# Kernel tuning notes

Measured on AMD Instinct MI355X. Metric: run time of the kernel, lower is better.

## Reference

```python
import jax, jax.numpy as jnp
import numpy as np

N = 20000
E = 320000
IN_C = 256
HID = 64
OUT_C = 64
NUM_LAYERS = 3
HEADS = 8


def setup_inputs() -> dict:
    key = jax.random.key(0)
    ks = jax.random.split(key, 12)
    s_in = 1.0 / np.sqrt(IN_C)
    s_h = 1.0 / np.sqrt(HID)
    inp = {
        "x": jax.random.normal(ks[0], (N, IN_C), dtype=jnp.float32),
        "edge_index": jax.random.randint(ks[1], (2, E), 0, N, dtype=jnp.int64),
        "lin1_w": jax.random.uniform(ks[2], (IN_C, HID), jnp.float32, -s_in, s_in),
        "lin1_b": jnp.zeros((HID,), jnp.float32),
        "wq": jax.random.uniform(ks[3], (NUM_LAYERS, HID, HID), jnp.float32, -s_h, s_h),
        "bq": jnp.zeros((NUM_LAYERS, HID), jnp.float32),
        "wk": jax.random.uniform(ks[4], (NUM_LAYERS, HID, HID), jnp.float32, -s_h, s_h),
        "bk": jnp.zeros((NUM_LAYERS, HID), jnp.float32),
        "wv": jax.random.uniform(ks[5], (NUM_LAYERS, HID, HID), jnp.float32, -s_h, s_h),
        "bv": jnp.zeros((NUM_LAYERS, HID), jnp.float32),
        "lin2_w": jax.random.uniform(ks[6], (HID, OUT_C), jnp.float32, -s_h, s_h),
        "lin2_b": jnp.zeros((OUT_C,), jnp.float32),
    }
    return inp


def reference(x, edge_index, lin1_w, lin1_b, wq, bq, wk, bk, wv, bv, lin2_w, lin2_b):
    n = x.shape[0]
    C = lin1_w.shape[1]
    d = C // HEADS  # per-head dim
    inv_sqrt_d = 1.0 / (d ** 0.5)

    # gcn_norm with self-loops (symmetric normalization, edge weights = 1)
    loop = jnp.arange(n, dtype=edge_index.dtype)
    row = jnp.concatenate([edge_index[0], loop])  # source j
    col = jnp.concatenate([edge_index[1], loop])  # target i
    deg = jax.ops.segment_sum(jnp.ones_like(col, dtype=x.dtype), col, num_segments=n)
    dinv = jnp.where(deg > 0, deg ** -0.5, 0.0)
    norm = dinv[row] * dinv[col]  # [E+N]

    # input projection (dropout inactive in eval mode)
    h = jax.nn.relu(x @ lin1_w + lin1_b)
    x_all = h[:, None, :]  # [N, 1, C] growing history

    for l in range(NUM_LAYERS):
        t = x_all.shape[1]
        # node-level projections (linear commutes with gather)
        q = x_all[:, -1] @ wq[l] + bq[l]                      # [N, C]
        k = jnp.einsum("ntc,cd->ntd", x_all, wk[l]) + bk[l]   # [N, t, C]
        v = jnp.einsum("ntc,cd->ntd", x_all, wv[l]) + bv[l]   # [N, t, C]
        # per-edge multi-head attention of target's latest repr over source history
        Qe = q[col].reshape(-1, HEADS, d)                      # [E', H, d]
        Ke = k[row].reshape(-1, t, HEADS, d)                   # [E', t, H, d]
        Ve = v[row].reshape(-1, t, HEADS, d)
        scores = jnp.einsum("ehd,ethd->eht", Qe, Ke) * inv_sqrt_d
        attn = jax.nn.softmax(scores, axis=-1)                 # [E', H, t]
        msg = jnp.einsum("eht,ethd->ehd", attn, Ve).reshape(-1, C)
        msg = msg * norm[:, None]
        out = jax.ops.segment_sum(msg, col, num_segments=n)    # sum aggregation
        out = jax.nn.relu(out)
        x_all = jnp.concatenate([x_all, out[:, None, :]], axis=1)

    logits = x_all[:, -1] @ lin2_w + lin2_b
    return jax.nn.log_softmax(logits, axis=1)
```

## Files before the change

### kernel.cpp

```cpp
#include <hip/hip_runtime.h>
#include <math.h>

#define HID 64
#define HEADS 8
#define ALD 72

typedef __attribute__((ext_vector_type(8))) short bf16x8;
typedef __attribute__((ext_vector_type(4))) float f32x4;

__device__ __forceinline__ unsigned short f2bf(float f) {
    union { float f; unsigned int u; } cv; cv.f = f;
    unsigned int u = cv.u;
    unsigned int r = (u + 0x7FFFu + ((u >> 16) & 1u)) >> 16;
    return (unsigned short)r;
}
__device__ __forceinline__ float bflo(unsigned int u) {
    union { unsigned int u; float f; } cv; cv.u = u << 16; return cv.f;
}
__device__ __forceinline__ float bfhi(unsigned int u) {
    union { unsigned int u; float f; } cv; cv.u = u & 0xFFFF0000u; return cv.f;
}
__device__ __forceinline__ unsigned relu_pk(unsigned u) {
    unsigned m = ((u & 0x8000u) ? 0u : 0xFFFFu) |
                 ((u & 0x80000000u) ? 0u : 0xFFFF0000u);
    return u & m;
}

__device__ __forceinline__ float dot2bf(unsigned a, unsigned b, float c) {
    float d;
    asm("v_dot2_f32_bf16 %0, %1, %2, %3" : "=v"(d) : "v"(a), "v"(b), "v"(c));
    return d;
}

__global__ void k_count(const int* __restrict__ col, int* __restrict__ counts, int E) {
    int e = blockIdx.x * blockDim.x + threadIdx.x;
    if (e < E) atomicAdd(&counts[col[e]], 1);
}

__device__ __forceinline__ void scan256_body(const int* __restrict__ counts,
                                             int* __restrict__ start,
                                             float* __restrict__ dinv, int n,
                                             int tid, int* sscan) {
    int lane = tid & 63, wvi = tid >> 6;
    int ipt = (n + 255) >> 8;
    int c0 = tid * ipt;
    int c1 = min(n, c0 + ipt);
    if (c0 > n) c0 = n;
    int s = 0;
    for (int i = c0; i < c1; ++i) s += counts[i];
    int x = s;
#pragma unroll
    for (int off = 1; off < 64; off <<= 1) {
        int y = __shfl_up(x, off);
        if (lane >= off) x += y;
    }
    if (lane == 63) sscan[wvi] = x;
    __syncthreads();
    if (tid == 0) {
        int r = 0;
#pragma unroll
        for (int i = 0; i < 4; ++i) { int t = sscan[i]; sscan[i + 4] = r; r += t; }
        start[n] = r;
    }
    __syncthreads();
    int run = sscan[wvi + 4] + (x - s);
    for (int i = c0; i < c1; ++i) {
        int v = counts[i];
        start[i] = run;
        dinv[i] = rsqrtf((float)(v + 1));
        run += v;
    }
}

__device__ __forceinline__ void stage_w_bf16(unsigned short* Wt,
                                             const float* __restrict__ w, int tid) {
    for (int idx = tid; idx < 1024; idx += 256) {
        int k = idx >> 4, n4 = (idx & 15) * 4;
        float4 wv = *(const float4*)&w[k * 64 + n4];
        Wt[(n4 + 0) * ALD + k] = f2bf(wv.x);
        Wt[(n4 + 1) * ALD + k] = f2bf(wv.y);
        Wt[(n4 + 2) * ALD + k] = f2bf(wv.z);
        Wt[(n4 + 3) * ALD + k] = f2bf(wv.w);
    }
}

__device__ __forceinline__ void mfma_step(const unsigned short* Alds,
                                          const unsigned short* Wt,
                                          int tid, f32x4 acc[4]) {
    int lane = tid & 63;
    int m0 = (tid >> 6) * 16;
    int c16 = lane & 15, quad = lane >> 4;
    const unsigned short* ar = &Alds[(m0 + c16) * ALD + quad * 8];
    bf16x8 a0 = *(const bf16x8*)ar;
    bf16x8 a1 = *(const bf16x8*)(ar + 32);
#pragma unroll
    for (int nt = 0; nt < 4; ++nt) {
        const unsigned short* br = &Wt[(nt * 16 + c16) * ALD + quad * 8];
        bf16x8 b0 = *(const bf16x8*)br;
        bf16x8 b1 = *(const bf16x8*)(br + 32);
        acc[nt] = __builtin_amdgcn_mfma_f32_16x16x32_bf16(a0, b0, acc[nt], 0, 0, 0);
        acc[nt] = __builtin_amdgcn_mfma_f32_16x16x32_bf16(a1, b1, acc[nt], 0, 0, 0);
    }
}

__device__ __forceinline__ void stage_tile_body(
    const unsigned short* __restrict__ src, const float* __restrict__ w,
    const float* __restrict__ b, float* __restrict__ qd,
    unsigned short* __restrict__ kvdst, int kv_stride, int kv_off, bool relu_in,
    int node0, int n, int tid, unsigned short* Alds, unsigned short* Wt) {
    stage_w_bf16(Wt, w, tid);
    for (int idx = tid; idx < 512; idx += 256) {
        int r = idx >> 3, seg = idx & 7;
        int node = node0 + r;
        uint4 u = make_uint4(0u, 0u, 0u, 0u);
        if (node < n) u = *(const uint4*)&src[(size_t)node * 64 + seg * 8];
        if (relu_in) {
            u.x = relu_pk(u.x); u.y = relu_pk(u.y);
            u.z = relu_pk(u.z); u.w = relu_pk(u.w);
        }
        *(uint4*)&Alds[r * ALD + seg * 8] = u;
    }
    __syncthreads();
    f32x4 acc[4];
#pragma unroll
    for (int nt = 0; nt < 4; ++nt) acc[nt] = (f32x4){0.f, 0.f, 0.f, 0.f};
    mfma_step(Alds, Wt, tid, acc);

    int lane = tid & 63;
    int m0 = (tid >> 6) * 16, c16 = lane & 15, quad = lane >> 4;
    float bias[4];
#pragma unroll
    for (int nt = 0; nt < 4; ++nt) bias[nt] = b[nt * 16 + c16];
    if (qd) {
#pragma unroll
        for (int i = 0; i < 4; ++i) {
            int node = node0 + m0 + quad * 4 + i;
            if (node < n) {
#pragma unroll
                for (int nt = 0; nt < 4; ++nt)
                    qd[(size_t)node * 64 + nt * 16 + c16] = acc[nt][i] + bias[nt];
            }
        }
    } else {
#pragma unroll
        for (int i = 0; i < 4; ++i) {
            int node = node0 + m0 + quad * 4 + i;
            if (node < n) {
#pragma unroll
                for (int nt = 0; nt < 4; ++nt)
                    kvdst[(size_t)node * kv_stride + kv_off + nt * 16 + c16] =
                        f2bf(acc[nt][i] + bias[nt]);
            }
        }
    }
}

__global__ __launch_bounds__(256, 4) void k_lin1_scan(
    const float* __restrict__ x, const float* __restrict__ w,
    const float* __restrict__ b, const float* __restrict__ wv0,
    const float* __restrict__ bv0, unsigned short* __restrict__ h,
    unsigned short* __restrict__ kv, const int* __restrict__ counts,
    int* __restrict__ startA, float* __restrict__ dinv, int n, int NT) {
    __shared__ __align__(16) unsigned short Alds[64 * ALD];
    __shared__ __align__(16) unsigned short Wt[64 * ALD];
    __shared__ int sscan[8];
    int tid = threadIdx.x;
    if (blockIdx.x == (unsigned)NT) {
        scan256_body(counts, startA, dinv, n, tid, sscan);
        return;
    }
    int node0 = blockIdx.x * 64;
    f32x4 acc[4];
#pragma unroll
    for (int nt = 0; nt < 4; ++nt) acc[nt] = (f32x4){0.f, 0.f, 0.f, 0.f};

    for (int kc = 0; kc < 256; kc += 64) {
        __syncthreads();
        stage_w_bf16(Wt, w + kc * 64, tid);
        for (int idx = tid; idx < 1024; idx += 256) {
            int r = idx >> 4, c4 = (idx & 15) * 4;
            int node = node0 + r;
            float4 v = make_float4(0.f, 0.f, 0.f, 0.f);
            if (node < n) v = *(const float4*)&x[(size_t)node * 256 + kc + c4];
            Alds[r * ALD + c4 + 0] = f2bf(v.x);
            Alds[r * ALD + c4 + 1] = f2bf(v.y);
            Alds[r * ALD + c4 + 2] = f2bf(v.z);
            Alds[r * ALD + c4 + 3] = f2bf(v.w);
        }
        __syncthreads();
        mfma_step(Alds, Wt, tid, acc);
    }
    int lane = tid & 63;
    int m0 = (tid >> 6) * 16, c16 = lane & 15, quad = lane >> 4;
    float bias[4];
#pragma unroll
    for (int nt = 0; nt < 4; ++nt) bias[nt] = b[nt * 16 + c16];

    __syncthreads();
    stage_w_bf16(Wt, wv0, tid);
#pragma unroll
    for (int i = 0; i < 4; ++i) {
        int row = m0 + quad * 4 + i;
        int node = node0 + row;
#pragma unroll
        for (int nt = 0; nt < 4; ++nt) {
            unsigned short hb = f2bf(fmaxf(acc[nt][i] + bias[nt], 0.f));
            Alds[row * ALD + nt * 16 + c16] = hb;
            if (node < n) h[(size_t)node * 64 + nt * 16 + c16] = hb;
        }
    }
    __syncthreads();
    f32x4 acc2[4];
#pragma unroll
    for (int nt = 0; nt < 4; ++nt) acc2[nt] = (f32x4){0.f, 0.f, 0.f, 0.f};
    mfma_step(Alds, Wt, tid, acc2);
    float bias2[4];
#pragma unroll
    for (int nt = 0; nt < 4; ++nt) bias2[nt] = bv0[nt * 16 + c16];
#pragma unroll
    for (int i = 0; i < 4; ++i) {
        int node = node0 + m0 + quad * 4 + i;
        if (node < n) {
#pragma unroll
            for (int nt = 0; nt < 4; ++nt)
                kv[(size_t)node * 64 + nt * 16 + c16] = f2bf(acc2[nt][i] + bias2[nt]);
        }
    }
}

__global__ __launch_bounds__(256, 4) void k_scatter_stage(
    const int* __restrict__ ei, const int* __restrict__ startA,
    int* __restrict__ counts, unsigned short* __restrict__ ebuf, int E, int nsb,
    const unsigned short* __restrict__ xs,
    const float* __restrict__ wk, const float* __restrict__ bk,
    const float* __restrict__ wv, const float* __restrict__ bv,
    unsigned short* __restrict__ kv1, unsigned short* __restrict__ kv2,
    int n, int NT) {
    __shared__ __align__(16) unsigned short Alds[64 * ALD];
    __shared__ __align__(16) unsigned short Wt[64 * ALD];
    int bx = blockIdx.x;
    if (bx < nsb) {
        int e = bx * 256 + threadIdx.x;
        if (e < E) {
            int r = ei[e], c = ei[E + e];
            int pos = startA[c] + atomicSub(&counts[c], 1) - 1;
            ebuf[pos] = (unsigned short)r;
        }
        return;
    }
    int t = bx - nsb;
    int j = t / NT, tile = t - j * NT;
    int layer = 1 + (j >> 1), isV = j & 1;
    const float* w = (isV ? wv : wk) + layer * 4096;
    const float* b = (isV ? bv : bk) + layer * 64;
    unsigned short* dst = (layer == 1) ? kv1 : kv2;
    int stride = (layer == 1) ? 256 : 384;
    int koff = isV ? 64 : 0;
    stage_tile_body(xs, w, b, nullptr, dst, stride, koff, false,
                    tile * 64, n, threadIdx.x, Alds, Wt);
}

__global__ __launch_bounds__(256, 4) void k_stage(
    const unsigned short* __restrict__ xs, size_t sstride,
    const float* __restrict__ wq, const float* __restrict__ bq,
    const float* __restrict__ wk, const float* __restrict__ bk,
    const float* __restrict__ wv, const float* __restrict__ bv,
    float* __restrict__ qbuf, unsigned short* __restrict__ kv1,
    unsigned short* __restrict__ kv2, int n, int phase) {
    __shared__ __align__(16) unsigned short Alds[64 * ALD];
    __shared__ __align__(16) unsigned short Wt[64 * ALD];
    int j = blockIdx.y;
    int layer, s, isV = 0, isQ = 0;
    if (phase == 1) {
        if (j < 4) { layer = 1 + (j >> 1); isV = j & 1; s = 1; }
        else       { layer = 1; isQ = 1; s = 1; }
    } else {
        if (j < 2) { layer = 2; isV = j; s = 2; }
        else       { layer = 2; isQ = 1; s = 2; }
    }
    const unsigned short* src = xs + (size_t)s * sstride;
    const float* w; const float* b;
    float* qd = nullptr; unsigned short* dst = nullptr;
    int stride = 0, koff = 0;
    if (isQ) {
        w = wq + layer * 4096; b = bq + layer * 64; qd = qbuf;
    } else {
        w = (isV ? wv : wk) + layer * 4096;
        b = (isV ? bv : bk) + layer * 64;
        dst = (layer == 1) ? kv1 : kv2;
        stride = (layer == 1) ? 256 : 384;
        koff = s * 128 + (isV ? 64 : 0);
    }
    stage_tile_body(src, w, b, qd, dst, stride, koff, true,
                    blockIdx.x * 64, n, threadIdx.x, Alds, Wt);
}

template <int T, bool FINAL>
__global__ __launch_bounds__(256) void k_attn(
    const int* __restrict__ start, const unsigned short* __restrict__ ebuf,
    const float* __restrict__ dinv, const float* __restrict__ q,
    const unsigned short* __restrict__ kv,
    const float* __restrict__ w2, const float* __restrict__ b2,
    unsigned short* __restrict__ outb, float* __restrict__ outf, int n) {
    const int KVS = (T == 1) ? 64 : T * 128;
    int node = (int)((blockIdx.x * (size_t)blockDim.x + threadIdx.x) >> 6);
    int lane = threadIdx.x & 63;
    if (node >= n) return;
    int g = lane >> 3;
    int cb = (lane & 7) * 8;

    unsigned qpk[4];
    if (T > 1) {
        const float isd = 0.35355339059327373f;
        float4 q0 = *(const float4*)&q[(size_t)node * 64 + cb];
        float4 q1 = *(const float4*)&q[(size_t)node * 64 + cb + 4];
        qpk[0] = ((unsigned)f2bf(q0.y * isd) << 16) | (unsigned)f2bf(q0.x * isd);
        qpk[1] = ((unsigned)f2bf(q0.w * isd) << 16) | (unsigned)f2bf(q0.z * isd);
        qpk[2] = ((unsigned)f2bf(q1.y * isd) << 16) | (unsigned)f2bf(q1.x * isd);
        qpk[3] = ((unsigned)f2bf(q1.w * isd) << 16) | (unsigned)f2bf(q1.z * isd);
    }
    float dc = dinv[node];
    int s0 = start[node];
    int cnt = start[node + 1] - s0 + 1;

    float acc[8];
#pragma unroll
    for (int k = 0; k < 8; ++k) acc[k] = 0.f;

    for (int base = 0; base < cnt; base += 8) {
        int idx = base + g;
        bool valid = idx < cnt;
        int r = node;
        if (valid && idx > 0) r = ebuf[s0 + idx - 1];
        float dr = valid ? dinv[r] : 0.f;
        const unsigned short* rkv = kv + (size_t)r * KVS;

        float cf[T];
        if (T > 1) {
            float sc[T];
            float m = -1e30f;
#pragma unroll
            for (int s = 0; s < T; ++s) {
                uint4 ku = *(const uint4*)&rkv[s * 128 + cb];
                float p = dot2bf(qpk[3], ku.w,
                          dot2bf(qpk[2], ku.z,
                          dot2bf(qpk[1], ku.y,
                          dot2bf(qpk[0], ku.x, 0.f))));
                sc[s] = p;
                m = fmaxf(m, p);
            }
            float denom = 0.f;
#pragma unroll
            for (int s = 0; s < T; ++s) { sc[s] = __expf(sc[s] - m); denom += sc[s]; }
            float w = dr / denom;
#pragma unroll
            for (int s = 0; s < T; ++s) cf[s] = w * sc[s];
        } else {
            cf[0] = dr;
        }
#pragma unroll
        for (int s = 0; s < T; ++s) {
            uint4 vu = *(const uint4*)&rkv[((T == 1) ? 0 : s * 128 + 64) + cb];
            float wv_ = cf[s];
            acc[0] += wv_ * bflo(vu.x); acc[1] += wv_ * bfhi(vu.x);
            acc[2] += wv_ * bflo(vu.y); acc[3] += wv_ * bfhi(vu.y);
            acc[4] += wv_ * bflo(vu.z); acc[5] += wv_ * bfhi(vu.z);
            acc[6] += wv_ * bflo(vu.w); acc[7] += wv_ * bfhi(vu.w);
        }
    }

#pragma unroll
    for (int off = 8; off < 64; off <<= 1) {
#pragma unroll
        for (int k = 0; k < 8; ++k) acc[k] += __shfl_xor(acc[k], off);
    }

    if (!FINAL) {
        if (g == 0) {
            ushort4 o0, o1;
            o0.x = f2bf(acc[0] * dc); o0.y = f2bf(acc[1] * dc);
            o0.z = f2bf(acc[2] * dc); o0.w = f2bf(acc[3] * dc);
            o1.x = f2bf(acc[4] * dc); o1.y = f2bf(acc[5] * dc);
            o1.z = f2bf(acc[6] * dc); o1.w = f2bf(acc[7] * dc);
            *(ushort4*)&outb[(size_t)node * 64 + cb] = o0;
            *(ushort4*)&outb[(size_t)node * 64 + cb + 4] = o1;
        }
    } else {
        float lg = b2[lane];
#pragma unroll
        for (int c = 0; c < 64; ++c) {
            float xc = fmaxf(__shfl(acc[c & 7], c >> 3) * dc, 0.f);
            lg += xc * w2[c * 64 + lane];
        }
        float mx = lg;
#pragma unroll
        for (int off = 1; off < 64; off <<= 1) mx = fmaxf(mx, __shfl_xor(mx, off));
        float e = __expf(lg - mx);
        float ssum = e;
#pragma unroll
        for (int off = 1; off < 64; off <<= 1) ssum += __shfl_xor(ssum, off);
        outf[(size_t)node * 64 + lane] = lg - mx - __logf(ssum);
    }
}

extern "C" void kernel_launch(void* const* d_in, const int* in_sizes, int n_in,
                              void* d_out, int out_size, void* d_ws, size_t ws_size,
                              hipStream_t stream) {
    const float* x  = (const float*)d_in[0];
    const int*   ei = (const int*)d_in[1];
    const float* w1 = (const float*)d_in[2];
    const float* b1 = (const float*)d_in[3];
    const float* wq = (const float*)d_in[4];
    const float* bq = (const float*)d_in[5];
    const float* wk = (const float*)d_in[6];
    const float* bk = (const float*)d_in[7];
    const float* wv = (const float*)d_in[8];
    const float* bv = (const float*)d_in[9];
    const float* w2 = (const float*)d_in[10];
    const float* b2 = (const float*)d_in[11];
    float* outp = (float*)d_out;

    int n = in_sizes[0] / 256;
    int E = in_sizes[1] / 2;

    float* ws = (float*)d_ws;
    size_t off = 0;
    float* dinv = ws + off; off += (size_t)n;
    float* qbuf = ws + off; off += (size_t)n * 64;
    unsigned short* xsU = (unsigned short*)(ws + off); off += (size_t)n * 96;
    unsigned short* kv0 = (unsigned short*)(ws + off); off += (size_t)n * 32;
    unsigned short* kv1 = (unsigned short*)(ws + off); off += (size_t)n * 128;
    unsigned short* kv2 = (unsigned short*)(ws + off); off += (size_t)n * 192;
    int* wsI    = (int*)(ws + off);
    int* counts = wsI;
    int* startA = wsI + n;
    unsigned short* ebuf = (unsigned short*)(wsI + 2 * n + 1);

    size_t sstride = (size_t)n * 64;
    int NT = (n + 63) / 64;
    int nsb = (E + 255) / 256;
    int attn_grid = (int)(((size_t)n * 64 + 255) / 256);

    hipMemsetAsync(counts, 0, (size_t)n * sizeof(int), stream);
    k_count<<<nsb, 256, 0, stream>>>(ei + E, counts, E);
    k_lin1_scan<<<NT + 1, 256, 0, stream>>>(x, w1, b1, wv, bv, xsU, kv0,
                                            counts, startA, dinv, n, NT);
    k_scatter_stage<<<nsb + 4 * NT, 256, 0, stream>>>(
        ei, startA, counts, ebuf, E, nsb, xsU, wk, bk, wv, bv, kv1, kv2, n, NT);
    k_attn<1, false><<<attn_grid, 256, 0, stream>>>(
        startA, ebuf, dinv, nullptr, kv0, nullptr, nullptr,
        xsU + sstride, nullptr, n);
    {
        dim3 grid(NT, 5);
        k_stage<<<grid, 256, 0, stream>>>(xsU, sstride, wq, bq, wk, bk, wv, bv,
                                          qbuf, kv1, kv2, n, 1);
    }
    k_attn<2, false><<<attn_grid, 256, 0, stream>>>(
        startA, ebuf, dinv, qbuf, kv1, nullptr, nullptr,
        xsU + 2 * sstride, nullptr, n);
    {
        dim3 grid(NT, 3);
        k_stage<<<grid, 256, 0, stream>>>(xsU, sstride, wq, bq, wk, bk, wv, bv,
                                          qbuf, kv1, kv2, n, 2);
    }
    k_attn<3, true><<<attn_grid, 256, 0, stream>>>(
        startA, ebuf, dinv, qbuf, kv2, w2, b2, nullptr, outp, n);
}
```

Baseline: 256.6 us.

## Fuse degree counting into lin1 kernel and move scan to a dedicated 1024-thread kernel

Degree counting now runs in extra blocks of the lin1 kernel, so the separate count launch goes away and counting overlaps with the projection GEMM. The prefix scan moves out of lin1 into its own single-block 1024-thread kernel, which cuts per-thread serial work and removes the scan block that previously sat on the lin1 tail. The weight staging index order is also changed so neighbouring threads read along k, which changes the global and LDS access pattern. This adds one kernel launch for the scan, in exchange for removing the count launch.

```diff
diff --git a/kernel.cpp b/kernel.cpp
--- a/kernel.cpp
+++ b/kernel.cpp
@@ -32,17 +32,13 @@
     return d;
 }
 
-__global__ void k_count(const int* __restrict__ col, int* __restrict__ counts, int E) {
-    int e = blockIdx.x * blockDim.x + threadIdx.x;
-    if (e < E) atomicAdd(&counts[col[e]], 1);
-}
-
-__device__ __forceinline__ void scan256_body(const int* __restrict__ counts,
-                                             int* __restrict__ start,
-                                             float* __restrict__ dinv, int n,
-                                             int tid, int* sscan) {
+__global__ __launch_bounds__(1024) void k_scan(const int* __restrict__ counts,
+                                               int* __restrict__ start,
+                                               float* __restrict__ dinv, int n) {
+    __shared__ int wsum[16];
+    int tid = threadIdx.x;
     int lane = tid & 63, wvi = tid >> 6;
-    int ipt = (n + 255) >> 8;
+    int ipt = (n + 1023) >> 10;
     int c0 = tid * ipt;
     int c1 = min(n, c0 + ipt);
     if (c0 > n) c0 = n;
@@ -54,28 +50,33 @@
         int y = __shfl_up(x, off);
         if (lane >= off) x += y;
     }
-    if (lane == 63) sscan[wvi] = x;
+    if (lane == 63) wsum[wvi] = x;
     __syncthreads();
-    if (tid == 0) {
-        int r = 0;
-#pragma unroll
-        for (int i = 0; i < 4; ++i) { int t = sscan[i]; sscan[i + 4] = r; r += t; }
-        start[n] = r;
+    if (wvi == 0 && lane < 16) {
+        int t2 = wsum[lane];
+#pragma unroll
+        for (int off = 1; off < 16; off <<= 1) {
+            int y = __shfl_up(t2, off);
+            if (lane >= off) t2 += y;
+        }
+        wsum[lane] = t2;
     }
     __syncthreads();
-    int run = sscan[wvi + 4] + (x - s);
+    int waveoff = (wvi > 0) ? wsum[wvi - 1] : 0;
+    int run = waveoff + x - s;
     for (int i = c0; i < c1; ++i) {
         int v = counts[i];
         start[i] = run;
         dinv[i] = rsqrtf((float)(v + 1));
         run += v;
     }
+    if (tid == 0) start[n] = wsum[15];
 }
 
 __device__ __forceinline__ void stage_w_bf16(unsigned short* Wt,
                                              const float* __restrict__ w, int tid) {
     for (int idx = tid; idx < 1024; idx += 256) {
-        int k = idx >> 4, n4 = (idx & 15) * 4;
+        int k = idx & 63, n4 = (idx >> 6) * 4;
         float4 wv = *(const float4*)&w[k * 64 + n4];
         Wt[(n4 + 0) * ALD + k] = f2bf(wv.x);
         Wt[(n4 + 1) * ALD + k] = f2bf(wv.y);
@@ -155,21 +156,22 @@
     }
 }
 
-__global__ __launch_bounds__(256, 4) void k_lin1_scan(
+__global__ __launch_bounds__(256, 4) void k_lin1cnt(
     const float* __restrict__ x, const float* __restrict__ w,
     const float* __restrict__ b, const float* __restrict__ wv0,
     const float* __restrict__ bv0, unsigned short* __restrict__ h,
-    unsigned short* __restrict__ kv, const int* __restrict__ counts,
-    int* __restrict__ startA, float* __restrict__ dinv, int n, int NT) {
+    unsigned short* __restrict__ kv, const int* __restrict__ ei,
+    int* __restrict__ counts, int E, int n, int NT) {
     __shared__ __align__(16) unsigned short Alds[64 * ALD];
     __shared__ __align__(16) unsigned short Wt[64 * ALD];
-    __shared__ int sscan[8];
     int tid = threadIdx.x;
-    if (blockIdx.x == (unsigned)NT) {
-        scan256_body(counts, startA, dinv, n, tid, sscan);
+    int bx = blockIdx.x;
+    if (bx >= NT) {
+        int e = (bx - NT) * 256 + tid;
+        if (e < E) atomicAdd(&counts[ei[E + e]], 1);
         return;
     }
-    int node0 = blockIdx.x * 64;
+    int node0 = bx * 64;
     f32x4 acc[4];
 #pragma unroll
     for (int nt = 0; nt < 4; ++nt) acc[nt] = (f32x4){0.f, 0.f, 0.f, 0.f};
@@ -442,9 +444,9 @@
     int attn_grid = (int)(((size_t)n * 64 + 255) / 256);
 
     hipMemsetAsync(counts, 0, (size_t)n * sizeof(int), stream);
-    k_count<<<nsb, 256, 0, stream>>>(ei + E, counts, E);
-    k_lin1_scan<<<NT + 1, 256, 0, stream>>>(x, w1, b1, wv, bv, xsU, kv0,
-                                            counts, startA, dinv, n, NT);
+    k_lin1cnt<<<NT + nsb, 256, 0, stream>>>(x, w1, b1, wv, bv, xsU, kv0,
+                                            ei, counts, E, n, NT);
+    k_scan<<<1, 1024, 0, stream>>>(counts, startA, dinv, n);
     k_scatter_stage<<<nsb + 4 * NT, 256, 0, stream>>>(
         ei, startA, counts, ebuf, E, nsb, xsU, wk, bk, wv, bv, kv1, kv2, n, NT);
     k_attn<1, false><<<attn_grid, 256, 0, stream>>>(
```

Result: no change. 259.0 us (+0.9%).
